# Kernel optimization log

Measured on AMD Instinct MI355X. Metric: run time of the kernel, lower is better.

The kernel has to match this reference:

```python
import jax, jax.numpy as jnp
import numpy as np

B, L, C, D, K = 32, 36864, 16, 512, 24


def setup_inputs() -> dict:
    key = jax.random.key(0)
    ks = jax.random.split(key, 5)
    x = jax.random.normal(ks[0], (B, L, C), jnp.float32)
    # offset-conv weights scaled small so predicted offsets are O(0.2) (kaiming-ish but tame)
    w_off = jax.random.normal(ks[1], (2 * K, C, K), jnp.float32) * 0.01
    b_off = jax.random.normal(ks[2], (2 * K,), jnp.float32) * 0.05
    w_def = jax.random.normal(ks[3], (D, C, K), jnp.float32) * (2.0 / (C * K)) ** 0.5
    b_def = jax.random.normal(ks[4], (D,), jnp.float32) * 0.05
    return {"x": x, "w_off": w_off, "b_off": b_off, "w_def": w_def, "b_def": b_def}


def reference(x, w_off, b_off, w_def, b_def):
    # x: [B, L, C] -> torch view [B, C, 1, L]; H == 1 throughout.
    Bn, Ln, Cn = x.shape
    twoK, _, Kn = w_off.shape
    Lout = Ln // Kn
    xc = jnp.transpose(x, (0, 2, 1))                 # [B, C, L]
    xk = xc.reshape(Bn, Cn, Lout, Kn)                # stride == kernel -> non-overlapping windows
    # offset conv: [B, 2K, Lout]
    off = jnp.einsum('bclk,ock->bol', xk, w_off) + b_off[None, :, None]
    off = off.reshape(Bn, Kn, 2, Lout)               # channel 2k -> dy, 2k+1 -> dx (torchvision layout)
    dy = jnp.transpose(off[:, :, 0, :], (0, 2, 1))   # [B, Lout, K]
    dx = jnp.transpose(off[:, :, 1, :], (0, 2, 1))   # [B, Lout, K]
    # sampling positions along width; base = w_out*K + k
    base = jnp.arange(Lout * Kn, dtype=x.dtype).reshape(Lout, Kn)
    px = base[None] + dx                             # [B, Lout, K]
    # height bilinear weight: with H=1, contribution at h=0 is max(0, 1-|dy|)
    wy = jnp.maximum(jnp.array(0, x.dtype), 1.0 - jnp.abs(dy))
    # width bilinear with zero padding (torchvision bilinear_interpolate semantics)
    valid = (px > -1.0) & (px < Ln)
    x0 = jnp.floor(px)
    lw = px - x0                                     # weight for right neighbor
    i0 = x0.astype(jnp.int32)
    i1 = i0 + 1
    m0 = (valid & (i0 >= 0) & (i0 < Ln)).astype(x.dtype)
    m1 = (valid & (i1 >= 0) & (i1 < Ln)).astype(x.dtype)
    i0c = jnp.broadcast_to(jnp.clip(i0, 0, Ln - 1).reshape(Bn, 1, Lout * Kn), (Bn, Cn, Lout * Kn))
    i1c = jnp.broadcast_to(jnp.clip(i1, 0, Ln - 1).reshape(Bn, 1, Lout * Kn), (Bn, Cn, Lout * Kn))
    v0 = jnp.take_along_axis(xc, i0c, axis=2).reshape(Bn, Cn, Lout, Kn)
    v1 = jnp.take_along_axis(xc, i1c, axis=2).reshape(Bn, Cn, Lout, Kn)
    val = (v0 * ((1.0 - lw) * m0)[:, None] + v1 * (lw * m1)[:, None]) * wy[:, None]  # [B,C,Lout,K]
    out = jnp.einsum('bclk,dck->bld', val, w_def) + b_def  # [B, Lout, D]
    return out
```

## Files before the change

kernel.cpp:

```cpp
#include <hip/hip_runtime.h>
#include <stdint.h>

#define BATCH 32
#define LLEN  36864
#define CCH   16
#define DOUT  512
#define KW    24
#define LOUT  1536
#define MROWS (BATCH * LOUT)
#define CK    384
#define TWOK  48

typedef float fx4 __attribute__((ext_vector_type(4)));
typedef float f32x4 __attribute__((ext_vector_type(4)));
typedef __bf16 bf16x8 __attribute__((ext_vector_type(8)));
typedef __bf16 bf16x4 __attribute__((ext_vector_type(4)));
typedef uint32_t u32x4 __attribute__((ext_vector_type(4)));

#define VMCNT(n)  asm volatile("s_waitcnt vmcnt(" #n ")" ::: "memory")
#define LGKMCNT0  asm volatile("s_waitcnt lgkmcnt(0)" ::: "memory")
#define SCHEDB    __builtin_amdgcn_sched_barrier(0)
#define SBAR      __builtin_amdgcn_s_barrier()

__device__ __forceinline__ void gload16(void* lds, const void* g)
{
    __builtin_amdgcn_global_load_lds(
        (const __attribute__((address_space(1))) uint32_t*)g,
        (__attribute__((address_space(3))) uint32_t*)lds, 16, 0, 0);
}

__global__ __launch_bounds__(256) void prep_kernel(
    const float* __restrict__ w_off, const float* __restrict__ w_def,
    __bf16* __restrict__ woff_b, __bf16* __restrict__ wdef_b)
{
    int idx = blockIdx.x * 256 + threadIdx.x;
    if (idx < TWOK * CK) {
        int o = idx / CK, rem = idx % CK;
        int k = rem >> 4, c = rem & 15;
        woff_b[idx] = (__bf16)w_off[o * CK + c * KW + k];
    }
    if (idx < DOUT * CK) {
        int d = idx / CK, rem = idx % CK;
        int k = rem >> 4, c = rem & 15;
        wdef_b[idx] = (__bf16)w_def[d * CK + c * KW + k];
    }
}

#define BM 96
#define BN 512
#define BK 64


__global__ __launch_bounds__(384) void k1_gather(
    const float* __restrict__ x, const __bf16* __restrict__ woff_b,
    const float* __restrict__ b_off, __bf16* __restrict__ A_ws, int mbase)
{
    __shared__ char smem[37632];
    __bf16* WoffS = (__bf16*)smem;
    float*  offS  = (float*)smem;

    const int t = threadIdx.x;
    const int mrel0 = blockIdx.x * BM;
    const int m0 = mbase + mrel0;
    const int wave = t >> 6, lane = t & 63;
    const int quad = lane >> 4, l16 = lane & 15;

    const int mloc = t >> 2, k4 = t & 3;
    const int Mrow = m0 + mloc;
    const int mrel = mrel0 + mloc;
    const int b    = m0 / LOUT;
    const int lb   = Mrow - b * LOUT;
    const float* xb = x + (size_t)b * LLEN * CCH;

#pragma unroll
    for (int i = 0; i < 6; ++i) {
        int q = t + 384 * i;
        int row = q / 48, cc = q - row * 48;
        *(u32x4*)&WoffS[row * 392 + cc * 8] =
            *(const u32x4*)&woff_b[row * CK + cc * 8];
    }
    __syncthreads();

    const float* xr = x + (size_t)(m0 + wave * 16 + l16) * CK;
    f32x4 oacc[3] = {};
#pragma unroll
    for (int ks = 0; ks < 12; ++ks) {
        int k0 = ks * 32 + quad * 8;
        fx4 a0 = *(const fx4*)&xr[k0];
        fx4 a1 = *(const fx4*)&xr[k0 + 4];
        bf16x8 af;
        af[0] = (__bf16)a0.x; af[1] = (__bf16)a0.y;
        af[2] = (__bf16)a0.z; af[3] = (__bf16)a0.w;
        af[4] = (__bf16)a1.x; af[5] = (__bf16)a1.y;
        af[6] = (__bf16)a1.z; af[7] = (__bf16)a1.w;
#pragma unroll
        for (int j = 0; j < 3; ++j) {
            bf16x8 bf = *(const bf16x8*)&WoffS[(j * 16 + l16) * 392 + k0];
            oacc[j] = __builtin_amdgcn_mfma_f32_16x16x32_bf16(af, bf, oacc[j], 0, 0, 0);
        }
    }
    float bo[3];
#pragma unroll
    for (int j = 0; j < 3; ++j) bo[j] = b_off[j * 16 + l16];
    __syncthreads();
#pragma unroll
    for (int j = 0; j < 3; ++j)
#pragma unroll
        for (int r = 0; r < 4; ++r)
            offS[(wave * 16 + quad * 4 + r) * 49 + j * 16 + l16] = oacc[j][r] + bo[j];
    __syncthreads();

    float dyv[6], dxv[6];
#pragma unroll
    for (int cc = 0; cc < 6; ++cc) {
        int kk = 4 * cc + k4;
        dyv[cc] = offS[mloc * 49 + 2 * kk];
        dxv[cc] = offS[mloc * 49 + 2 * kk + 1];
    }

    for (int cc = 0; cc < 6; ++cc) {
        int kk = 4 * cc + k4;
        float dy = dyv[cc], dx = dxv[cc];
        float wy  = fmaxf(0.f, 1.f - fabsf(dy));
        float px  = (float)(lb * KW + kk) + dx;
        float x0f = floorf(px);
        float lw  = px - x0f;
        int   i0  = (int)x0f;
        bool valid = (px > -1.0f) && (px < (float)LLEN);
        float w0 = (valid && i0 >= 0)         ? (1.f - lw) * wy : 0.f;
        float w1 = (valid && (i0 + 1) < LLEN) ? lw * wy         : 0.f;
        int i0c = min(max(i0, 0), LLEN - 1);
        int i1c = min(max(i0 + 1, 0), LLEN - 1);
        const fx4* p0 = (const fx4*)&xb[(size_t)i0c * CCH];
        const fx4* p1 = (const fx4*)&xb[(size_t)i1c * CCH];
        fx4 g0[4], g1[4];
#pragma unroll
        for (int q = 0; q < 4; ++q) { g0[q] = p0[q]; g1[q] = p1[q]; }
        bf16x8 oa, ob;
#pragma unroll
        for (int q = 0; q < 2; ++q) {
            fx4 v0 = g0[q], v1 = g1[q];
            oa[q * 4 + 0] = (__bf16)(w0 * v0.x + w1 * v1.x);
            oa[q * 4 + 1] = (__bf16)(w0 * v0.y + w1 * v1.y);
            oa[q * 4 + 2] = (__bf16)(w0 * v0.z + w1 * v1.z);
            oa[q * 4 + 3] = (__bf16)(w0 * v0.w + w1 * v1.w);
        }
#pragma unroll
        for (int q = 0; q < 2; ++q) {
            fx4 v0 = g0[q + 2], v1 = g1[q + 2];
            ob[q * 4 + 0] = (__bf16)(w0 * v0.x + w1 * v1.x);
            ob[q * 4 + 1] = (__bf16)(w0 * v0.y + w1 * v1.y);
            ob[q * 4 + 2] = (__bf16)(w0 * v0.z + w1 * v1.z);
            ob[q * 4 + 3] = (__bf16)(w0 * v0.w + w1 * v1.w);
        }
        __bf16* dst = A_ws + (size_t)mrel * CK + kk * 16;
        *(bf16x8*)dst       = oa;
        *(bf16x8*)(dst + 8) = ob;
    }
}

__global__ __launch_bounds__(512) void k2_gemm(
    const __bf16* __restrict__ A_ws, const __bf16* __restrict__ Bw,
    const float* __restrict__ bias, float* __restrict__ out, int mbase)
{
    __shared__ char smem[77824];
    __bf16* As0 = (__bf16*)smem;
    __bf16* As1 = (__bf16*)(smem + 6144);
    __bf16* Bs0 = (__bf16*)(smem + 12288);
    __bf16* Bs1 = (__bf16*)(smem + 45056);

    const int t = threadIdx.x;
    const int mrel0 = blockIdx.x * BM;
    const int wave = t >> 6, lane = t & 63;
    const int quad = lane >> 4, l16 = lane & 15;
    const int wr = wave >> 2, wc = wave & 3;

    auto dma = [&](int p, __bf16* AsB, __bf16* BsB) {
#pragma unroll
        for (int it = 0; it < 4; ++it) {
            int q = it * 512 + t;
            int c = q >> 2, s = q & 3;
            int ss = s ^ ((c >> 1) & 3);
            gload16(&BsB[q * 8], Bw + (size_t)c * CK + p * 32 + ss * 8);
        }
        if (t < 384) {
            int row = t >> 2, g = t & 3;
            int gg = g ^ ((row >> 1) & 3);
            gload16(&AsB[t * 8],
                    A_ws + (size_t)(mrel0 + row) * CK + p * 32 + gg * 8);
        }
    };

    f32x4 acc[3][8] = {};

    auto mfma_phase = [&](const __bf16* AsB, const __bf16* BsB) {
        bf16x8 af[3], bfr[8];
#pragma unroll
        for (int i = 0; i < 3; ++i) {
            int row = wr * 48 + i * 16 + l16;
            af[i] = *(const bf16x8*)&AsB[row * 32 + ((quad ^ ((row >> 1) & 3)) * 8)];
        }
#pragma unroll
        for (int j = 0; j < 8; ++j) {
            int col = wc * 128 + j * 16 + l16;
            bfr[j] = *(const bf16x8*)&BsB[col * 32 + ((quad ^ ((col >> 1) & 3)) * 8)];
        }
#pragma unroll
        for (int i = 0; i < 3; ++i)
#pragma unroll
            for (int j = 0; j < 8; ++j)
                acc[i][j] = __builtin_amdgcn_mfma_f32_16x16x32_bf16(
                    af[i], bfr[j], acc[i][j], 0, 0, 0);
    };

    dma(0, As0, Bs0);
#pragma unroll
    for (int p = 0; p < 12; ++p) {
        __bf16* Ac = (p & 1) ? As1 : As0;
        __bf16* Bc = (p & 1) ? Bs1 : Bs0;
        __bf16* An = (p & 1) ? As0 : As1;
        __bf16* Bn = (p & 1) ? Bs0 : Bs1;
        if (p < 11) dma(p + 1, An, Bn);
        SCHEDB;
        if (p < 11) { if (wave < 6) { VMCNT(5); } else { VMCNT(4); } }
        else        { VMCNT(0); }
        SCHEDB;
        SBAR;
        SCHEDB;
        __builtin_amdgcn_s_setprio(1);
        mfma_phase(Ac, Bc);
        __builtin_amdgcn_s_setprio(0);
        SCHEDB;
        SBAR;
        SCHEDB;
    }

#pragma unroll
    for (int j = 0; j < 8; ++j) {
        int col = wc * 128 + j * 16 + l16;
        float bj = bias[col];
#pragma unroll
        for (int i = 0; i < 3; ++i) {
            int rowb = mbase + mrel0 + wr * 48 + i * 16 + quad * 4;
#pragma unroll
            for (int r = 0; r < 4; ++r)
                out[(size_t)(rowb + r) * DOUT + col] = acc[i][j][r] + bj;
        }
    }
}

__global__ __launch_bounds__(512) void gemm_fused(
    const float* __restrict__ x, const __bf16* __restrict__ woff_b,
    const float* __restrict__ b_off, const __bf16* __restrict__ Bw,
    const float* __restrict__ bias, float* __restrict__ out)
{
    __shared__ char smem[77824];
    __bf16* As  = (__bf16*)smem;
    __bf16* Bs0 = (__bf16*)(smem + 12288);
    __bf16* Bs1 = (__bf16*)(smem + 45056);
    __bf16* WoffS = (__bf16*)smem;
    float*  offS  = (float*)(smem + 45056);

    const int t = threadIdx.x;
    const int m0 = blockIdx.x * BM;
    const int wave = t >> 6, lane = t & 63;
    const int quad = lane >> 4, l16 = lane & 15;
    const int wr = wave >> 2, wc = wave & 3;

    const int mloc = t >> 2, k4 = t & 3;
    const int Mrow = m0 + mloc;
    const int b    = m0 / LOUT;
    const int lb   = Mrow - b * LOUT;
    const float* xb = x + (size_t)b * LLEN * CCH;

#pragma unroll
    for (int i = 0; i < 5; ++i) {
        int q = t + 512 * i;
        if (q < 2304) {
            int row = q / 48, cc = q - row * 48;
            *(u32x4*)&WoffS[row * 392 + cc * 8] =
                *(const u32x4*)&woff_b[row * CK + cc * 8];
        }
    }
    __syncthreads();

    if (wave < 6) {
        const float* xr = x + (size_t)(m0 + wave * 16 + l16) * CK;
        f32x4 oacc[3] = {};
#pragma unroll
        for (int ks = 0; ks < 12; ++ks) {
            int k0 = ks * 32 + quad * 8;
            fx4 a0 = *(const fx4*)&xr[k0];
            fx4 a1 = *(const fx4*)&xr[k0 + 4];
            bf16x8 af;
            af[0] = (__bf16)a0.x; af[1] = (__bf16)a0.y;
            af[2] = (__bf16)a0.z; af[3] = (__bf16)a0.w;
            af[4] = (__bf16)a1.x; af[5] = (__bf16)a1.y;
            af[6] = (__bf16)a1.z; af[7] = (__bf16)a1.w;
#pragma unroll
            for (int j = 0; j < 3; ++j) {
                bf16x8 bf = *(const bf16x8*)&WoffS[(j * 16 + l16) * 392 + k0];
                oacc[j] = __builtin_amdgcn_mfma_f32_16x16x32_bf16(af, bf, oacc[j], 0, 0, 0);
            }
        }
        float bo[3];
#pragma unroll
        for (int j = 0; j < 3; ++j) bo[j] = b_off[j * 16 + l16];
#pragma unroll
        for (int j = 0; j < 3; ++j)
#pragma unroll
            for (int r = 0; r < 4; ++r)
                offS[(wave * 16 + quad * 4 + r) * 49 + j * 16 + l16] = oacc[j][r] + bo[j];
    }
    __syncthreads();

    uint32_t dxyr[6];
    if (t < 4 * BM) {
#pragma unroll
        for (int cc = 0; cc < 6; ++cc) {
            int kk = 4 * cc + k4;
            float dy = offS[mloc * 49 + 2 * kk];
            float dx = offS[mloc * 49 + 2 * kk + 1];
            union { __bf16 h[2]; uint32_t u; } p;
            p.h[0] = (__bf16)dy; p.h[1] = (__bf16)dx;
            dxyr[cc] = p.u;
        }
    }

    f32x4 acc[3][8] = {};
    fx4 g0[4], g1[4];
    float w0, w1;

    auto load_pair = [&](uint32_t pk, int kk) {
        union { uint32_t u; __bf16 h[2]; } p; p.u = pk;
        float dy = (float)p.h[0], dx = (float)p.h[1];
        float wy  = fmaxf(0.f, 1.f - fabsf(dy));
        float px  = (float)(lb * KW + kk) + dx;
        float x0f = floorf(px);
        float lw  = px - x0f;
        int   i0  = (int)x0f;
        bool valid = (px > -1.0f) && (px < (float)LLEN);
        w0 = (valid && i0 >= 0)         ? (1.f - lw) * wy : 0.f;
        w1 = (valid && (i0 + 1) < LLEN) ? lw * wy         : 0.f;
        int i0c = min(max(i0, 0), LLEN - 1);
        int i1c = min(max(i0 + 1, 0), LLEN - 1);
        const fx4* p0 = (const fx4*)&xb[(size_t)i0c * CCH];
        const fx4* p1 = (const fx4*)&xb[(size_t)i1c * CCH];
#pragma unroll
        for (int q = 0; q < 4; ++q) { g0[q] = p0[q]; g1[q] = p1[q]; }
    };

    auto dma_phase = [&](int ph, __bf16* buf) {
#pragma unroll
        for (int it = 0; it < 4; ++it) {
            int q = it * 512 + t;
            int c = q >> 2, s = q & 3;
            int ss = s ^ ((c >> 1) & 3);
            gload16(&buf[q * 8], Bw + (size_t)c * CK + ph * 32 + ss * 8);
        }
    };

    auto mfma_phase = [&](int ks, const __bf16* Bsb) {
        bf16x8 af[3], bfr[8];
#pragma unroll
        for (int i = 0; i < 3; ++i) {
            int row = wr * 48 + i * 16 + l16;
            af[i] = *(const bf16x8*)&As[row * BK + (((ks * 4 + quad) ^ (row & 7)) * 8)];
        }
#pragma unroll
        for (int j = 0; j < 8; ++j) {
            int col = wc * 128 + j * 16 + l16;
            bfr[j] = *(const bf16x8*)&Bsb[col * 32 + ((quad ^ ((col >> 1) & 3)) * 8)];
        }
#pragma unroll
        for (int i = 0; i < 3; ++i)
#pragma unroll
            for (int j = 0; j < 8; ++j)
                acc[i][j] = __builtin_amdgcn_mfma_f32_16x16x32_bf16(
                    af[i], bfr[j], acc[i][j], 0, 0, 0);
    };

    if (t < 4 * BM) load_pair(dxyr[0], k4);
    SCHEDB;
    dma_phase(0, Bs0);
    SCHEDB;

#pragma unroll
    for (int cc = 0; cc < 6; ++cc) {
        SBAR;
        SCHEDB;
        VMCNT(4);
        SCHEDB;
        if (t < 4 * BM) {
            bf16x8 oa, ob;
#pragma unroll
            for (int q = 0; q < 2; ++q) {
                fx4 v0 = g0[q], v1 = g1[q];
                oa[q * 4 + 0] = (__bf16)(w0 * v0.x + w1 * v1.x);
                oa[q * 4 + 1] = (__bf16)(w0 * v0.y + w1 * v1.y);
                oa[q * 4 + 2] = (__bf16)(w0 * v0.z + w1 * v1.z);
                oa[q * 4 + 3] = (__bf16)(w0 * v0.w + w1 * v1.w);
            }
#pragma unroll
            for (int q = 0; q < 2; ++q) {
                fx4 v0 = g0[q + 2], v1 = g1[q + 2];
                ob[q * 4 + 0] = (__bf16)(w0 * v0.x + w1 * v1.x);
                ob[q * 4 + 1] = (__bf16)(w0 * v0.y + w1 * v1.y);
                ob[q * 4 + 2] = (__bf16)(w0 * v0.z + w1 * v1.z);
                ob[q * 4 + 3] = (__bf16)(w0 * v0.w + w1 * v1.w);
            }
            int g = 2 * k4;
            *(bf16x8*)&As[mloc * BK + ((g ^ (mloc & 7)) * 8)]       = oa;
            *(bf16x8*)&As[mloc * BK + (((g + 1) ^ (mloc & 7)) * 8)] = ob;
        }
        SCHEDB;
        dma_phase(2 * cc + 1, Bs1);
        SCHEDB;
        if (cc + 1 < 6 && t < 4 * BM)
            load_pair(dxyr[cc + 1], 4 * (cc + 1) + k4);
        SCHEDB;
        LGKMCNT0;
        SCHEDB;
        SBAR;
        SCHEDB;
        if (cc < 5) { if (wave < 6) { VMCNT(12); } else { VMCNT(4); } }
        else        { VMCNT(4); }
        SCHEDB;
        SBAR;
        SCHEDB;
        __builtin_amdgcn_s_setprio(1);
        mfma_phase(0, Bs0);
        __builtin_amdgcn_s_setprio(0);
        SCHEDB;
        if (cc < 5) { if (wave < 6) { VMCNT(8); } else { VMCNT(0); } }
        else        { VMCNT(0); }
        SCHEDB;
        SBAR;
        SCHEDB;
        if (cc < 5) dma_phase(2 * cc + 2, Bs0);
        SCHEDB;
        __builtin_amdgcn_s_setprio(1);
        mfma_phase(1, Bs1);
        __builtin_amdgcn_s_setprio(0);
        SCHEDB;
    }

#pragma unroll
    for (int j = 0; j < 8; ++j) {
        int col = wc * 128 + j * 16 + l16;
        float bj = bias[col];
#pragma unroll
        for (int i = 0; i < 3; ++i) {
            int rowb = m0 + wr * 48 + i * 16 + quad * 4;
#pragma unroll
            for (int r = 0; r < 4; ++r)
                out[(size_t)(rowb + r) * DOUT + col] = acc[i][j][r] + bj;
        }
    }
}

extern "C" void kernel_launch(void* const* d_in, const int* in_sizes, int n_in,
                              void* d_out, int out_size, void* d_ws, size_t ws_size,
                              hipStream_t stream)
{
    const float* x     = (const float*)d_in[0];
    const float* w_off = (const float*)d_in[1];
    const float* b_off = (const float*)d_in[2];
    const float* w_def = (const float*)d_in[3];
    const float* b_def = (const float*)d_in[4];
    float* out = (float*)d_out;

    char* ws = (char*)d_ws;
    __bf16* wdef_b = (__bf16*)ws;
    __bf16* woff_b = (__bf16*)(ws + 393216);
    __bf16* A_ws   = (__bf16*)(ws + 430080);

    prep_kernel<<<768, 256, 0, stream>>>(w_off, w_def, woff_b, wdef_b);

    const size_t afull = (size_t)MROWS * CK * 2;
    int S = -1;
    for (int s = 1; s <= 32; s <<= 1) {
        if (430080 + afull / s <= ws_size) { S = s; break; }
    }
    if (S > 0) {
        int rows = MROWS / S;
        int nb   = rows / BM;
        for (int c = 0; c < S; ++c) {
            int mb = c * rows;
            k1_gather<<<nb, 384, 0, stream>>>(x, woff_b, b_off, A_ws, mb);
            k2_gemm<<<nb, 512, 0, stream>>>(A_ws, wdef_b, b_def, out, mb);
        }
    } else {
        gemm_fused<<<MROWS / BM, 512, 0, stream>>>(x, woff_b, b_off, wdef_b, b_def, out);
    }
}
```

Measured before the change: 216.3 us.

## Retile k2 GEMM to 64x128 tiles with 256-thread blocks for occupancy

The split-path GEMM goes from 96x512 output tiles on 512-thread blocks to 64x128 tiles on 256-thread blocks, with four N-tiles per M-tile and LDS cut to 24KB so several blocks fit per CU. The launch bounds allow four blocks per multiprocessor, and the trailing barrier of the last stage is dropped. The goal is more resident waves and better latency hiding for the memory-bound GEMM. The cost is that each A tile is now loaded from global memory four times and each block does less MFMA work per tile load.

```diff
diff --git a/kernel.cpp b/kernel.cpp
--- a/kernel.cpp
+++ b/kernel.cpp
@@ -159,56 +159,60 @@
     }
 }
 
-__global__ __launch_bounds__(512) void k2_gemm(
+__global__ __launch_bounds__(256, 4) void k2_gemm(
     const __bf16* __restrict__ A_ws, const __bf16* __restrict__ Bw,
     const float* __restrict__ bias, float* __restrict__ out, int mbase)
 {
-    __shared__ char smem[77824];
+    __shared__ char smem[24576];
     __bf16* As0 = (__bf16*)smem;
-    __bf16* As1 = (__bf16*)(smem + 6144);
-    __bf16* Bs0 = (__bf16*)(smem + 12288);
-    __bf16* Bs1 = (__bf16*)(smem + 45056);
+    __bf16* Bs0 = (__bf16*)(smem + 4096);
+    __bf16* As1 = (__bf16*)(smem + 12288);
+    __bf16* Bs1 = (__bf16*)(smem + 16384);
 
     const int t = threadIdx.x;
-    const int mrel0 = blockIdx.x * BM;
+    const int mtile = blockIdx.x >> 2;
+    const int n0 = (blockIdx.x & 3) * 128;
+    const int m0rel = mtile * 64;
     const int wave = t >> 6, lane = t & 63;
     const int quad = lane >> 4, l16 = lane & 15;
-    const int wr = wave >> 2, wc = wave & 3;
+    const int wr = wave >> 1, wc = wave & 1;
 
     auto dma = [&](int p, __bf16* AsB, __bf16* BsB) {
 #pragma unroll
-        for (int it = 0; it < 4; ++it) {
-            int q = it * 512 + t;
-            int c = q >> 2, s = q & 3;
-            int ss = s ^ ((c >> 1) & 3);
-            gload16(&BsB[q * 8], Bw + (size_t)c * CK + p * 32 + ss * 8);
-        }
-        if (t < 384) {
-            int row = t >> 2, g = t & 3;
-            int gg = g ^ ((row >> 1) & 3);
-            gload16(&AsB[t * 8],
-                    A_ws + (size_t)(mrel0 + row) * CK + p * 32 + gg * 8);
+        for (int it = 0; it < 3; ++it) {
+            int q = it * 256 + t;
+            if (q < 512) {
+                int c = q >> 2, s = q & 3;
+                int ss = s ^ ((c >> 1) & 3);
+                gload16(&BsB[q * 8], Bw + (size_t)(n0 + c) * CK + p * 32 + ss * 8);
+            } else {
+                int q2 = q - 512;
+                int row = q2 >> 2, s = q2 & 3;
+                int ss = s ^ ((row >> 1) & 3);
+                gload16(&AsB[q2 * 8],
+                        A_ws + (size_t)(m0rel + row) * CK + p * 32 + ss * 8);
+            }
         }
     };
 
-    f32x4 acc[3][8] = {};
+    f32x4 acc[2][4] = {};
 
     auto mfma_phase = [&](const __bf16* AsB, const __bf16* BsB) {
-        bf16x8 af[3], bfr[8];
-#pragma unroll
-        for (int i = 0; i < 3; ++i) {
-            int row = wr * 48 + i * 16 + l16;
+        bf16x8 af[2], bfr[4];
+#pragma unroll
+        for (int i = 0; i < 2; ++i) {
+            int row = wr * 32 + i * 16 + l16;
             af[i] = *(const bf16x8*)&AsB[row * 32 + ((quad ^ ((row >> 1) & 3)) * 8)];
         }
 #pragma unroll
-        for (int j = 0; j < 8; ++j) {
-            int col = wc * 128 + j * 16 + l16;
+        for (int j = 0; j < 4; ++j) {
+            int col = wc * 64 + j * 16 + l16;
             bfr[j] = *(const bf16x8*)&BsB[col * 32 + ((quad ^ ((col >> 1) & 3)) * 8)];
         }
 #pragma unroll
-        for (int i = 0; i < 3; ++i)
-#pragma unroll
-            for (int j = 0; j < 8; ++j)
+        for (int i = 0; i < 2; ++i)
+#pragma unroll
+            for (int j = 0; j < 4; ++j)
                 acc[i][j] = __builtin_amdgcn_mfma_f32_16x16x32_bf16(
                     af[i], bfr[j], acc[i][j], 0, 0, 0);
     };
@@ -222,7 +226,7 @@
         __bf16* Bn = (p & 1) ? Bs0 : Bs1;
         if (p < 11) dma(p + 1, An, Bn);
         SCHEDB;
-        if (p < 11) { if (wave < 6) { VMCNT(5); } else { VMCNT(4); } }
+        if (p < 11) { VMCNT(3); }
         else        { VMCNT(0); }
         SCHEDB;
         SBAR;
@@ -231,17 +235,16 @@
         mfma_phase(Ac, Bc);
         __builtin_amdgcn_s_setprio(0);
         SCHEDB;
-        SBAR;
-        SCHEDB;
-    }
-
-#pragma unroll
-    for (int j = 0; j < 8; ++j) {
-        int col = wc * 128 + j * 16 + l16;
+        if (p < 11) { SBAR; SCHEDB; }
+    }
+
+#pragma unroll
+    for (int j = 0; j < 4; ++j) {
+        int col = n0 + wc * 64 + j * 16 + l16;
         float bj = bias[col];
 #pragma unroll
-        for (int i = 0; i < 3; ++i) {
-            int rowb = mbase + mrel0 + wr * 48 + i * 16 + quad * 4;
+        for (int i = 0; i < 2; ++i) {
+            int rowb = mbase + m0rel + wr * 32 + i * 16 + quad * 4;
 #pragma unroll
             for (int r = 0; r < 4; ++r)
                 out[(size_t)(rowb + r) * DOUT + col] = acc[i][j][r] + bj;
@@ -484,11 +487,10 @@
     }
     if (S > 0) {
         int rows = MROWS / S;
-        int nb   = rows / BM;
         for (int c = 0; c < S; ++c) {
             int mb = c * rows;
-            k1_gather<<<nb, 384, 0, stream>>>(x, woff_b, b_off, A_ws, mb);
-            k2_gemm<<<nb, 512, 0, stream>>>(A_ws, wdef_b, b_def, out, mb);
+            k1_gather<<<rows / BM, 384, 0, stream>>>(x, woff_b, b_off, A_ws, mb);
+            k2_gemm<<<(rows / 64) * 4, 256, 0, stream>>>(A_ws, wdef_b, b_def, out, mb);
         }
     } else {
         gemm_fused<<<MROWS / BM, 512, 0, stream>>>(x, woff_b, b_off, wdef_b, b_def, out);
```

New measurement: 215.7 us. About the same (-0.3%).
